# Kernel tuning notes

Measured on AMD Instinct MI355X. Metric: run time of the kernel, lower is better.

Reference implementation:

```python
import jax, jax.numpy as jnp
import numpy as np

B, L, LH, D, H = 32, 512, 2048, 1024, 4
DK = D // H  # dot-attn head dim
NEG = -1e9


def _ln(x, g, b, eps=1e-5):
    m = x.mean(-1, keepdims=True)
    v = ((x - m) ** 2).mean(-1, keepdims=True)
    return (x - m) / jnp.sqrt(v + eps) * g + b


def setup_inputs() -> dict:
    key = jax.random.key(0)
    ks = jax.random.split(key, 16)
    s = 0.05
    inp = {
        "seq_emb": jax.random.normal(ks[0], (B, L, D), jnp.float32),
        "seq_mask": jnp.ones((B, L), jnp.float32),
        "his_seq_emb": jax.random.normal(ks[1], (B, LH, D), jnp.float32),
        "his_seq_mask": jnp.ones((B, LH), jnp.float32),
        # dot-product MHA (bias=True)
        "sa_wq": jax.random.normal(ks[2], (D, D), jnp.float32) * s,
        "sa_bq": jnp.zeros((D,), jnp.float32),
        "sa_wk": jax.random.normal(ks[3], (D, D), jnp.float32) * s,
        "sa_bk": jnp.zeros((D,), jnp.float32),
        "sa_wv": jax.random.normal(ks[4], (D, D), jnp.float32) * s,
        "sa_bv": jnp.zeros((D,), jnp.float32),
        "sa_wo": jax.random.normal(ks[5], (D, D), jnp.float32) * s,
        "sa_bo": jnp.zeros((D,), jnp.float32),
        # short LayerNorm
        "sn_g": jnp.ones((D,), jnp.float32),
        "sn_b": jnp.zeros((D,), jnp.float32),
        # additive MHA (h=1, bias=False)
        "aa_wq": jax.random.normal(ks[6], (D, D), jnp.float32) * s,
        "aa_wk": jax.random.normal(ks[7], (D, D), jnp.float32) * s,
        "aa_wv": jax.random.normal(ks[8], (D, D), jnp.float32) * s,
        "aa_wo": jax.random.normal(ks[9], (D, D), jnp.float32) * s,
        "aa_wa": jax.random.normal(ks[10], (D,), jnp.float32) * s,
        # long LayerNorm
        "ln_g": jnp.ones((D,), jnp.float32),
        "ln_b": jnp.zeros((D,), jnp.float32),
    }
    return inp


def reference(seq_emb, seq_mask, his_seq_emb, his_seq_mask,
              sa_wq, sa_bq, sa_wk, sa_bk, sa_wv, sa_bv, sa_wo, sa_bo,
              sn_g, sn_b, aa_wq, aa_wk, aa_wv, aa_wo, aa_wa, ln_g, ln_b):
    # ---- dot-product self attention over seq_emb (dropout = eval/no-op) ----
    def split_heads(x):  # (B,L,D) -> (B,H,L,DK)
        return x.reshape(B, -1, H, DK).transpose(0, 2, 1, 3)

    q = split_heads(seq_emb @ sa_wq + sa_bq)
    k = split_heads(seq_emb @ sa_wk + sa_bk)
    v = split_heads(seq_emb @ sa_wv + sa_bv)
    scores = jnp.einsum('bhqd,bhkd->bhqk', q, k) / jnp.sqrt(jnp.float32(DK))
    scores = jnp.where(seq_mask[:, None, None, :] == 0, NEG, scores)
    p_attn = jax.nn.softmax(scores, axis=-1)  # (B,H,L,L)
    ctx = jnp.einsum('bhqk,bhkd->bhqd', p_attn, v)
    ctx = ctx.transpose(0, 2, 1, 3).reshape(B, L, D)
    sa_out = ctx @ sa_wo + sa_bo

    poi_attn = _ln(sa_out, sn_g, sn_b) * seq_mask[:, :, None]
    poi_hidden = poi_attn.mean(axis=1, keepdims=True)  # (B,1,D)

    # ---- additive (Bahdanau) attention, h=1, Lq=1 ----
    aq = poi_hidden @ aa_wq        # (B,1,D)
    ak = his_seq_emb @ aa_wk       # (B,LH,D)
    av = his_seq_emb @ aa_wv       # (B,LH,D)
    feats = jnp.tanh(aq[:, :, None, :] + ak[:, None, :, :])  # (B,1,LH,D)
    a_scores = jnp.einsum('bqkd,d->bqk', feats, aa_wa)        # (B,1,LH)
    a_scores = jnp.where(his_seq_mask[:, None, :] == 0, NEG, a_scores)
    a_w = jax.nn.softmax(a_scores, axis=-1)
    a_ctx = jnp.einsum('bqk,bkd->bqd', a_w, av)               # (B,1,D)
    aa_out = a_ctx @ aa_wo

    his_poi_hidden = poi_hidden + _ln(aa_out, ln_g, ln_b)     # (B,1,D)

    attn_weight = p_attn[:, 0, :, :]                          # (B,L,L)
    seq_hidden = jnp.concatenate([poi_hidden, his_poi_hidden], axis=-1)[:, 0, :]  # (B,2D)
    return seq_hidden, attn_weight
```

## Files before the change

### kernel.cpp

```cpp
#include <hip/hip_runtime.h>

#define NEGV (-1000000000.0f)

typedef __attribute__((ext_vector_type(8))) short sh8;
typedef __attribute__((ext_vector_type(4))) short sh4;
typedef __attribute__((ext_vector_type(8))) __bf16 bf16x8;
typedef __attribute__((ext_vector_type(4))) float f32x4;

__device__ __forceinline__ float b2f(unsigned short u) {
  unsigned v = ((unsigned)u) << 16;
  return __builtin_bit_cast(float, v);
}
__device__ __forceinline__ unsigned short f2b(float f) {
  unsigned x = __builtin_bit_cast(unsigned, f);
  unsigned r = (x + 0x7fffu + ((x >> 16) & 1u)) >> 16;
  return (unsigned short)r;
}
__device__ __forceinline__ void g2l16(const void* g, void* l) {
  __builtin_amdgcn_global_load_lds((const __attribute__((address_space(1))) unsigned int*)g,
                                   (__attribute__((address_space(3))) unsigned int*)l, 16, 0, 0);
}
__device__ __forceinline__ f32x4 mfma16(bf16x8 a, bf16x8 b, f32x4 c) {
  return __builtin_amdgcn_mfma_f32_16x16x32_bf16(a, b, c, 0, 0, 0);
}
__device__ __forceinline__ float fast_tanh(float x) {
  x = fminf(fmaxf(x, -15.f), 15.f);
  float e = __expf(2.f * x);
  return (e - 1.f) / (e + 1.f);
}

__global__ void cvt_bf16(const float* __restrict__ src, unsigned short* __restrict__ dst, int n4) {
  int i = blockIdx.x * blockDim.x + threadIdx.x;
  int stride = gridDim.x * blockDim.x;
  for (; i < n4; i += stride) {
    float4 v = ((const float4*)src)[i];
    sh4 o;
    o[0] = (short)f2b(v.x); o[1] = (short)f2b(v.y);
    o[2] = (short)f2b(v.z); o[3] = (short)f2b(v.w);
    ((sh4*)dst)[i] = o;
  }
}

__global__ void tcvt(const float* __restrict__ src, unsigned short* __restrict__ dst) {
  __shared__ float tile[64][65];
  int bx = blockIdx.x, by = blockIdx.y;
  int tx = threadIdx.x & 63, ty = threadIdx.x >> 6;
#pragma unroll
  for (int i = 0; i < 16; ++i) {
    int r = i * 4 + ty;
    tile[r][tx] = src[(size_t)(by * 64 + r) * 1024 + bx * 64 + tx];
  }
  __syncthreads();
#pragma unroll
  for (int i = 0; i < 16; ++i) {
    int r = i * 4 + ty;
    dst[(size_t)(bx * 64 + r) * 1024 + by * 64 + tx] = f2b(tile[tx][r]);
  }
}

template<int EPI>
__global__ __launch_bounds__(256, 2)
void gemm128(const unsigned short* __restrict__ A, const unsigned short* __restrict__ Bt,
             const float* __restrict__ bias, unsigned short* __restrict__ C,
             const float* __restrict__ aq, const float* __restrict__ wa,
             float* __restrict__ sc)
{
  __shared__ unsigned short ldsA[128 * 32];
  __shared__ unsigned short ldsB[128 * 32];
  const int tid = threadIdx.x;
  const int w = tid >> 6, l = tid & 63;
  const int wr = w >> 1, wc = w & 1;
  const int lr = l & 15, lk8 = (l >> 4) * 8;
  const int wg = blockIdx.x;
  const int cpx = gridDim.x >> 3;
  const int wgid = (wg & 7) * cpx + (wg >> 3);
  const int bx = wgid & 7, by = wgid >> 3;
  const int m0 = by * 128;
  const int n0 = bx * 128;

  f32x4 acc[4][4] = {};

  const int srow = tid >> 2;
  const int scol = (tid & 3) * 8;
  const unsigned short* gA0 = A + (size_t)(m0 + srow) * 1024 + scol;
  const unsigned short* gB0 = Bt + (size_t)(n0 + srow) * 1024 + scol;
  unsigned short* lA = &ldsA[w * 512];
  unsigned short* lB = &ldsB[w * 512];

  for (int kt = 0; kt < 32; ++kt) {
    const int k0 = kt * 32;
    g2l16(gA0 + k0, lA);
    g2l16(gA0 + 64 * 1024 + k0, lA + 2048);
    g2l16(gB0 + k0, lB);
    g2l16(gB0 + 64 * 1024 + k0, lB + 2048);
    __syncthreads();
    bf16x8 af[4], bf[4];
#pragma unroll
    for (int i = 0; i < 4; ++i)
      af[i] = *(const bf16x8*)&ldsA[(wr * 64 + i * 16 + lr) * 32 + lk8];
#pragma unroll
    for (int j = 0; j < 4; ++j)
      bf[j] = *(const bf16x8*)&ldsB[(wc * 64 + j * 16 + lr) * 32 + lk8];
#pragma unroll
    for (int i = 0; i < 4; ++i)
#pragma unroll
      for (int j = 0; j < 4; ++j)
        acc[i][j] = mfma16(af[i], bf[j], acc[i][j]);
    __syncthreads();
  }

  if (EPI == 0) {
#pragma unroll
    for (int j = 0; j < 4; ++j) {
      int col = n0 + wc * 64 + j * 16 + lr;
      float bv = bias[col];
#pragma unroll
      for (int i = 0; i < 4; ++i) {
        int rowb = m0 + wr * 64 + i * 16 + (l >> 4) * 4;
#pragma unroll
        for (int r = 0; r < 4; ++r)
          C[(size_t)(rowb + r) * 1024 + col] = f2b(acc[i][j][r] + bv);
      }
    }
  } else if (EPI == 1) {
#pragma unroll
    for (int j = 0; j < 4; ++j) {
      int col = n0 + wc * 64 + j * 16 + lr;
      float bv = bias[col];
      int h = col >> 8, d = col & 255;
#pragma unroll
      for (int i = 0; i < 4; ++i) {
        int rowb = m0 + wr * 64 + i * 16 + (l >> 4) * 4;
        int bb = rowb >> 9, ll = rowb & 511;
        size_t base = ((size_t)(bb * 4 + h) * 256 + d) * 512 + ll;
#pragma unroll
        for (int r = 0; r < 4; ++r)
          C[base + r] = f2b(acc[i][j][r] + bv);
      }
    }
  } else {
    const int bb = m0 >> 11;
#pragma unroll
    for (int i = 0; i < 4; ++i) {
      float rp[4] = {0.f, 0.f, 0.f, 0.f};
#pragma unroll
      for (int j = 0; j < 4; ++j) {
        int col = n0 + wc * 64 + j * 16 + lr;
        float wav = wa[col];
        float aqv = aq[bb * 1024 + col];
#pragma unroll
        for (int r = 0; r < 4; ++r)
          rp[r] += wav * fast_tanh(acc[i][j][r] + aqv);
      }
#pragma unroll
      for (int off = 1; off < 16; off <<= 1)
#pragma unroll
        for (int r = 0; r < 4; ++r)
          rp[r] += __shfl_xor(rp[r], off, 64);
      if (lr == 0) {
        int rowb = m0 + wr * 64 + i * 16 + (l >> 4) * 4;
#pragma unroll
        for (int r = 0; r < 4; ++r)
          atomicAdd(&sc[rowb + r], rp[r]);
      }
    }
  }
}

__global__ __launch_bounds__(256, 4)
void attn_kernel(const unsigned short* __restrict__ q, const unsigned short* __restrict__ k,
                 const unsigned short* __restrict__ vT, const float* __restrict__ seq_mask,
                 unsigned short* __restrict__ ctx, float* __restrict__ attn_out)
{
  __shared__ char smem[34304];
  unsigned short* Qs = (unsigned short*)smem;
  unsigned short* Ps = (unsigned short*)smem;
  float* redm = (float*)(smem + 33280);
  float* reds = (float*)(smem + 33792);
  const int t = threadIdx.x, w = t >> 6, l = t & 63;
  const int lr = l & 15, g = l >> 4, lk8 = g * 8;
  const int wg = blockIdx.x;
  const int wgid = (wg & 7) * 256 + (wg >> 3);
  const int qt = wgid & 15, bh = wgid >> 4;
  const int h = bh & 3, b = bh >> 2;
  const int l0 = qt * 32;

  for (int idx = t; idx < 32 * 32; idx += 256) {
    int r = idx >> 5, ch = (idx & 31) * 8;
    *(sh8*)&Qs[r * 264 + ch] =
        *(const sh8*)&q[((size_t)(b * 512 + l0 + r)) * 1024 + h * 256 + ch];
  }
  __syncthreads();

  f32x4 accs[2][8] = {};
  const unsigned short* kbase = k + ((size_t)b * 512) * 1024 + h * 256;
#pragma unroll
  for (int ds = 0; ds < 8; ++ds) {
    int d0 = ds * 32;
    bf16x8 a0 = *(const bf16x8*)&Qs[lr * 264 + d0 + lk8];
    bf16x8 a1 = *(const bf16x8*)&Qs[(16 + lr) * 264 + d0 + lk8];
#pragma unroll
    for (int j = 0; j < 8; ++j) {
      int kj = w * 128 + j * 16 + lr;
      bf16x8 bb = *(const bf16x8*)&kbase[(size_t)kj * 1024 + d0 + lk8];
      accs[0][j] = mfma16(a0, bb, accs[0][j]);
      accs[1][j] = mfma16(a1, bb, accs[1][j]);
    }
  }

#pragma unroll
  for (int j = 0; j < 8; ++j) {
    int col = w * 128 + j * 16 + lr;
    float mv = seq_mask[b * 512 + col];
    bool msk = (mv == 0.f);
#pragma unroll
    for (int i = 0; i < 2; ++i)
#pragma unroll
      for (int r = 0; r < 4; ++r)
        accs[i][j][r] = msk ? NEGV : accs[i][j][r] * 0.0625f;
  }

  float mx[2][4], sm[2][4];
#pragma unroll
  for (int i = 0; i < 2; ++i)
#pragma unroll
    for (int r = 0; r < 4; ++r) {
      float m = accs[i][0][r];
#pragma unroll
      for (int j = 1; j < 8; ++j) m = fmaxf(m, accs[i][j][r]);
      mx[i][r] = m;
    }
#pragma unroll
  for (int off = 1; off < 16; off <<= 1)
#pragma unroll
    for (int i = 0; i < 2; ++i)
#pragma unroll
      for (int r = 0; r < 4; ++r)
        mx[i][r] = fmaxf(mx[i][r], __shfl_xor(mx[i][r], off, 64));
  if (lr == 0) {
#pragma unroll
    for (int i = 0; i < 2; ++i)
#pragma unroll
      for (int r = 0; r < 4; ++r)
        redm[w * 32 + i * 16 + g * 4 + r] = mx[i][r];
  }
  __syncthreads();
#pragma unroll
  for (int i = 0; i < 2; ++i)
#pragma unroll
    for (int r = 0; r < 4; ++r) {
      int row = i * 16 + g * 4 + r;
      mx[i][r] = fmaxf(fmaxf(redm[row], redm[32 + row]),
                       fmaxf(redm[64 + row], redm[96 + row]));
      sm[i][r] = 0.f;
    }

#pragma unroll
  for (int i = 0; i < 2; ++i)
#pragma unroll
    for (int j = 0; j < 8; ++j)
#pragma unroll
      for (int r = 0; r < 4; ++r) {
        float p = __expf(accs[i][j][r] - mx[i][r]);
        accs[i][j][r] = p;
        sm[i][r] += p;
      }
#pragma unroll
  for (int off = 1; off < 16; off <<= 1)
#pragma unroll
    for (int i = 0; i < 2; ++i)
#pragma unroll
      for (int r = 0; r < 4; ++r)
        sm[i][r] += __shfl_xor(sm[i][r], off, 64);
  if (lr == 0) {
#pragma unroll
    for (int i = 0; i < 2; ++i)
#pragma unroll
      for (int r = 0; r < 4; ++r)
        reds[w * 32 + i * 16 + g * 4 + r] = sm[i][r];
  }
  __syncthreads();
#pragma unroll
  for (int i = 0; i < 2; ++i)
#pragma unroll
    for (int r = 0; r < 4; ++r) {
      int row = i * 16 + g * 4 + r;
      float s = reds[row] + reds[32 + row] + reds[64 + row] + reds[96 + row];
      sm[i][r] = 1.f / s;
    }

#pragma unroll
  for (int i = 0; i < 2; ++i)
#pragma unroll
    for (int j = 0; j < 8; ++j) {
      int col = w * 128 + j * 16 + lr;
#pragma unroll
      for (int r = 0; r < 4; ++r) {
        int row = i * 16 + g * 4 + r;
        float pn = accs[i][j][r] * sm[i][r];
        Ps[row * 520 + col] = f2b(pn);
        if (h == 0)
          attn_out[((size_t)(b * 512 + l0 + row)) * 512 + col] = pn;
      }
    }
  __syncthreads();

  f32x4 acco[2][4] = {};
  const unsigned short* vbase = vT + ((size_t)(b * 4 + h)) * 256 * 512;
#pragma unroll
  for (int ks = 0; ks < 16; ++ks) {
    int kj0 = ks * 32;
    bf16x8 a0 = *(const bf16x8*)&Ps[lr * 520 + kj0 + lk8];
    bf16x8 a1 = *(const bf16x8*)&Ps[(16 + lr) * 520 + kj0 + lk8];
#pragma unroll
    for (int j = 0; j < 4; ++j) {
      int d = w * 64 + j * 16 + lr;
      bf16x8 bb = *(const bf16x8*)&vbase[(size_t)d * 512 + kj0 + lk8];
      acco[0][j] = mfma16(a0, bb, acco[0][j]);
      acco[1][j] = mfma16(a1, bb, acco[1][j]);
    }
  }
#pragma unroll
  for (int i = 0; i < 2; ++i)
#pragma unroll
    for (int j = 0; j < 4; ++j) {
      int col = w * 64 + j * 16 + lr;
#pragma unroll
      for (int r = 0; r < 4; ++r) {
        int row = i * 16 + g * 4 + r;
        ctx[((size_t)(b * 512 + l0 + row)) * 1024 + h * 256 + col] = f2b(acco[i][j][r]);
      }
    }
}

__global__ __launch_bounds__(256)
void ln_mean(const unsigned short* __restrict__ sa, const float* __restrict__ g,
             const float* __restrict__ bt, const float* __restrict__ mask,
             float* __restrict__ poi_sum)
{
  const int b = blockIdx.y, ch = blockIdx.x;
  const int t = threadIdx.x, w = t >> 6, l = t & 63;
  float gg[16], bb[16];
#pragma unroll
  for (int j = 0; j < 16; ++j) { gg[j] = g[l * 16 + j]; bb[j] = bt[l * 16 + j]; }
  float accv[16];
#pragma unroll
  for (int j = 0; j < 16; ++j) accv[j] = 0.f;
  for (int rr = 0; rr < 16; ++rr) {
    int row = ch * 64 + w * 16 + rr;
    const unsigned short* rp = sa + ((size_t)(b * 512 + row)) * 1024 + l * 16;
    float x[16];
    sh8 v0 = *(const sh8*)rp;
    sh8 v1 = *(const sh8*)(rp + 8);
#pragma unroll
    for (int j = 0; j < 8; ++j) {
      x[j] = b2f((unsigned short)v0[j]);
      x[8 + j] = b2f((unsigned short)v1[j]);
    }
    float s = 0.f, s2 = 0.f;
#pragma unroll
    for (int j = 0; j < 16; ++j) { s += x[j]; s2 += x[j] * x[j]; }
#pragma unroll
    for (int off = 1; off < 64; off <<= 1) {
      s += __shfl_xor(s, off, 64);
      s2 += __shfl_xor(s2, off, 64);
    }
    float mean = s * (1.f / 1024.f);
    float var = s2 * (1.f / 1024.f) - mean * mean;
    float rinv = rsqrtf(var + 1e-5f);
    float mk = mask[b * 512 + row];
#pragma unroll
    for (int j = 0; j < 16; ++j) accv[j] += ((x[j] - mean) * rinv * gg[j] + bb[j]) * mk;
  }
#pragma unroll
  for (int j = 0; j < 16; ++j) atomicAdd(&poi_sum[b * 1024 + l * 16 + j], accv[j]);
}

__global__ void finalize_poi(const float* __restrict__ ps, float* __restrict__ poi) {
  int i = blockIdx.x * 256 + threadIdx.x;
  if (i < 32 * 1024) poi[i] = ps[i] * (1.f / 512.f);
}

__global__ __launch_bounds__(256)
void gemv32(const float* __restrict__ in, const float* __restrict__ W, float* __restrict__ out)
{
  const int b = blockIdx.y;
  const int n = blockIdx.x * 256 + threadIdx.x;
  const float* ib = in + b * 1024;
  float acc = 0.f;
  for (int d = 0; d < 1024; d += 4) {
    acc += ib[d]     * W[(size_t)d * 1024 + n]
         + ib[d + 1] * W[(size_t)(d + 1) * 1024 + n]
         + ib[d + 2] * W[(size_t)(d + 2) * 1024 + n]
         + ib[d + 3] * W[(size_t)(d + 3) * 1024 + n];
  }
  out[b * 1024 + n] = acc;
}

__global__ __launch_bounds__(256)
void softmax_his(float* __restrict__ sc, const float* __restrict__ mask)
{
  __shared__ float red[4];
  const int b = blockIdx.x, t = threadIdx.x, w = t >> 6, l = t & 63;
  float v[8];
  float mx = -3.0e38f;
#pragma unroll
  for (int i = 0; i < 8; ++i) {
    int kk = t + i * 256;
    float s = (mask[b * 2048 + kk] == 0.f) ? NEGV : sc[b * 2048 + kk];
    v[i] = s;
    mx = fmaxf(mx, s);
  }
#pragma unroll
  for (int off = 1; off < 64; off <<= 1) mx = fmaxf(mx, __shfl_xor(mx, off, 64));
  if (l == 0) red[w] = mx;
  __syncthreads();
  mx = fmaxf(fmaxf(red[0], red[1]), fmaxf(red[2], red[3]));
  float sum = 0.f;
#pragma unroll
  for (int i = 0; i < 8; ++i) { v[i] = __expf(v[i] - mx); sum += v[i]; }
#pragma unroll
  for (int off = 1; off < 64; off <<= 1) sum += __shfl_xor(sum, off, 64);
  __syncthreads();
  if (l == 0) red[w] = sum;
  __syncthreads();
  sum = red[0] + red[1] + red[2] + red[3];
  float inv = 1.f / sum;
#pragma unroll
  for (int i = 0; i < 8; ++i) sc[b * 2048 + t + i * 256] = v[i] * inv;
}

__global__ __launch_bounds__(256)
void hw_kernel(const float* __restrict__ aw, const unsigned short* __restrict__ his,
               float* __restrict__ hw)
{
  const int b = blockIdx.y, kc = blockIdx.x, t = threadIdx.x;
  const int cb = t * 4;
  float a0 = 0.f, a1 = 0.f, a2 = 0.f, a3 = 0.f;
  for (int kk = 0; kk < 256; ++kk) {
    int k = kc * 256 + kk;
    float wg = aw[b * 2048 + k];
    sh4 vv = *(const sh4*)&his[((size_t)(b * 2048 + k)) * 1024 + cb];
    a0 += wg * b2f((unsigned short)vv[0]);
    a1 += wg * b2f((unsigned short)vv[1]);
    a2 += wg * b2f((unsigned short)vv[2]);
    a3 += wg * b2f((unsigned short)vv[3]);
  }
  atomicAdd(&hw[b * 1024 + cb + 0], a0);
  atomicAdd(&hw[b * 1024 + cb + 1], a1);
  atomicAdd(&hw[b * 1024 + cb + 2], a2);
  atomicAdd(&hw[b * 1024 + cb + 3], a3);
}

__global__ __launch_bounds__(256)
void final_kernel(const float* __restrict__ aa_out, const float* __restrict__ g,
                  const float* __restrict__ bt, const float* __restrict__ poi,
                  float* __restrict__ out)
{
  __shared__ float r1[4], r2[4];
  const int b = blockIdx.x, t = threadIdx.x, w = t >> 6, l = t & 63;
  float x[4];
#pragma unroll
  for (int j = 0; j < 4; ++j) x[j] = aa_out[b * 1024 + t * 4 + j];
  float s = 0.f, s2 = 0.f;
#pragma unroll
  for (int j = 0; j < 4; ++j) { s += x[j]; s2 += x[j] * x[j]; }
#pragma unroll
  for (int off = 1; off < 64; off <<= 1) {
    s += __shfl_xor(s, off, 64);
    s2 += __shfl_xor(s2, off, 64);
  }
  if (l == 0) { r1[w] = s; r2[w] = s2; }
  __syncthreads();
  s = r1[0] + r1[1] + r1[2] + r1[3];
  s2 = r2[0] + r2[1] + r2[2] + r2[3];
  float mean = s * (1.f / 1024.f);
  float var = s2 * (1.f / 1024.f) - mean * mean;
  float rinv = rsqrtf(var + 1e-5f);
#pragma unroll
  for (int j = 0; j < 4; ++j) {
    int c = t * 4 + j;
    float lnv = (x[j] - mean) * rinv * g[c] + bt[c];
    float pv = poi[b * 1024 + c];
    out[b * 2048 + c] = pv;
    out[b * 2048 + 1024 + c] = pv + lnv;
  }
}

extern "C" void kernel_launch(void* const* d_in, const int* in_sizes, int n_in,
                              void* d_out, int out_size, void* d_ws, size_t ws_size,
                              hipStream_t stream)
{
  const float* seq_emb  = (const float*)d_in[0];
  const float* seq_mask = (const float*)d_in[1];
  const float* his_emb  = (const float*)d_in[2];
  const float* his_mask = (const float*)d_in[3];
  const float* sa_wq = (const float*)d_in[4];
  const float* sa_bq = (const float*)d_in[5];
  const float* sa_wk = (const float*)d_in[6];
  const float* sa_bk = (const float*)d_in[7];
  const float* sa_wv = (const float*)d_in[8];
  const float* sa_bv = (const float*)d_in[9];
  const float* sa_wo = (const float*)d_in[10];
  const float* sa_bo = (const float*)d_in[11];
  const float* sn_g  = (const float*)d_in[12];
  const float* sn_b  = (const float*)d_in[13];
  const float* aa_wq = (const float*)d_in[14];
  const float* aa_wk = (const float*)d_in[15];
  const float* aa_wv = (const float*)d_in[16];
  const float* aa_wo = (const float*)d_in[17];
  const float* aa_wa = (const float*)d_in[18];
  const float* ln_g  = (const float*)d_in[19];
  const float* ln_b  = (const float*)d_in[20];
  float* out = (float*)d_out;

  char* p = (char*)d_ws;
  size_t off = 0;
  auto alloc = [&](size_t bytes) -> void* {
    void* r = p + off;
    off += (bytes + 255) & ~(size_t)255;
    return r;
  };
  unsigned short* seqb = (unsigned short*)alloc((size_t)16384 * 1024 * 2);
  unsigned short* hisb = (unsigned short*)alloc((size_t)65536 * 1024 * 2);
  unsigned short* wqT  = (unsigned short*)alloc((size_t)1024 * 1024 * 2);
  unsigned short* wkT  = (unsigned short*)alloc((size_t)1024 * 1024 * 2);
  unsigned short* wvT  = (unsigned short*)alloc((size_t)1024 * 1024 * 2);
  unsigned short* woT  = (unsigned short*)alloc((size_t)1024 * 1024 * 2);
  unsigned short* awkT = (unsigned short*)alloc((size_t)1024 * 1024 * 2);
  unsigned short* qb   = (unsigned short*)alloc((size_t)16384 * 1024 * 2);
  unsigned short* kb   = (unsigned short*)alloc((size_t)16384 * 1024 * 2);
  unsigned short* vTb  = (unsigned short*)alloc((size_t)16384 * 1024 * 2);
  unsigned short* ctxb = (unsigned short*)alloc((size_t)16384 * 1024 * 2);
  unsigned short* saob = (unsigned short*)alloc((size_t)16384 * 1024 * 2);
  float* poi_sum = (float*)alloc((size_t)32 * 1024 * 4);
  float* poi     = (float*)alloc((size_t)32 * 1024 * 4);
  float* aqb     = (float*)alloc((size_t)32 * 1024 * 4);
  float* ascore  = (float*)alloc((size_t)32 * 2048 * 4);
  float* hwb     = (float*)alloc((size_t)32 * 1024 * 4);
  float* actx    = (float*)alloc((size_t)32 * 1024 * 4);
  float* aaout   = (float*)alloc((size_t)32 * 1024 * 4);
  if (off > ws_size) return;

  hipMemsetAsync(poi_sum, 0, (size_t)32 * 1024 * 4, stream);
  hipMemsetAsync(ascore, 0, (size_t)32 * 2048 * 4, stream);
  hipMemsetAsync(hwb, 0, (size_t)32 * 1024 * 4, stream);

  cvt_bf16<<<2048, 256, 0, stream>>>(seq_emb, seqb, 16384 * 1024 / 4);
  cvt_bf16<<<2048, 256, 0, stream>>>(his_emb, hisb, 65536 * 1024 / 4);
  dim3 tg(16, 16);
  tcvt<<<tg, 256, 0, stream>>>(sa_wq, wqT);
  tcvt<<<tg, 256, 0, stream>>>(sa_wk, wkT);
  tcvt<<<tg, 256, 0, stream>>>(sa_wv, wvT);
  tcvt<<<tg, 256, 0, stream>>>(sa_wo, woT);
  tcvt<<<tg, 256, 0, stream>>>(aa_wk, awkT);

  gemm128<0><<<1024, 256, 0, stream>>>(seqb, wqT, sa_bq, qb, nullptr, nullptr, nullptr);
  gemm128<0><<<1024, 256, 0, stream>>>(seqb, wkT, sa_bk, kb, nullptr, nullptr, nullptr);
  gemm128<1><<<1024, 256, 0, stream>>>(seqb, wvT, sa_bv, vTb, nullptr, nullptr, nullptr);

  attn_kernel<<<2048, 256, 0, stream>>>(qb, kb, vTb, seq_mask, ctxb, out + 65536);

  gemm128<0><<<1024, 256, 0, stream>>>(ctxb, woT, sa_bo, saob, nullptr, nullptr, nullptr);
  ln_mean<<<dim3(8, 32), 256, 0, stream>>>(saob, sn_g, sn_b, seq_mask, poi_sum);
  finalize_poi<<<128, 256, 0, stream>>>(poi_sum, poi);
  gemv32<<<dim3(4, 32), 256, 0, stream>>>(poi, aa_wq, aqb);

  gemm128<2><<<4096, 256, 0, stream>>>(hisb, awkT, nullptr, nullptr, aqb, aa_wa, ascore);
  softmax_his<<<32, 256, 0, stream>>>(ascore, his_mask);
  hw_kernel<<<dim3(8, 32), 256, 0, stream>>>(ascore, hisb, hwb);
  gemv32<<<dim3(4, 32), 256, 0, stream>>>(hwb, aa_wv, actx);
  gemv32<<<dim3(4, 32), 256, 0, stream>>>(actx, aa_wo, aaout);
  final_kernel<<<32, 256, 0, stream>>>(aaout, ln_g, ln_b, poi, out);
}
```

Baseline: 823.2 us.

## Replace 128x128 GEMM with pipelined 256x256 tile kernel and fuse QKV projections

Replaces the 128x128-tile, 256-thread GEMM with a 256x256-tile, 512-thread kernel that keeps a 4-stage LDS ring, loading two k-steps ahead. Loads are interleaved with MFMA phases using split barriers, explicit waitcnt and setprio. The Q/K/V weights are concatenated so one launch computes all three projections. The goal is more data reuse per tile, hiding global-load latency, and fewer launches. In exchange it uses 128KB of LDS at one block per CU, and the hand-managed vmcnt and barrier logic is fragile.

```diff
diff --git a/kernel.cpp b/kernel.cpp
--- a/kernel.cpp
+++ b/kernel.cpp
@@ -59,93 +59,154 @@
 }
 
 template<int EPI>
-__global__ __launch_bounds__(256, 2)
-void gemm128(const unsigned short* __restrict__ A, const unsigned short* __restrict__ Bt,
-             const float* __restrict__ bias, unsigned short* __restrict__ C,
+__global__ __launch_bounds__(512, 1)
+void gemm256(const unsigned short* __restrict__ A, const unsigned short* __restrict__ Bt,
+             int nbx,
+             const float* __restrict__ b0, const float* __restrict__ b1,
+             const float* __restrict__ b2,
+             unsigned short* __restrict__ O0, unsigned short* __restrict__ O1,
+             unsigned short* __restrict__ O2,
              const float* __restrict__ aq, const float* __restrict__ wa,
              float* __restrict__ sc)
 {
-  __shared__ unsigned short ldsA[128 * 32];
-  __shared__ unsigned short ldsB[128 * 32];
+  __shared__ char lds[131072];
   const int tid = threadIdx.x;
   const int w = tid >> 6, l = tid & 63;
-  const int wr = w >> 1, wc = w & 1;
-  const int lr = l & 15, lk8 = (l >> 4) * 8;
+  const int wm = w >> 2, wn = w & 3;
+  const int lr = l & 15, g = l >> 4;
+  const int kg16 = g * 16;
+
   const int wg = blockIdx.x;
   const int cpx = gridDim.x >> 3;
   const int wgid = (wg & 7) * cpx + (wg >> 3);
-  const int bx = wgid & 7, by = wgid >> 3;
-  const int m0 = by * 128;
-  const int n0 = bx * 128;
-
-  f32x4 acc[4][4] = {};
-
-  const int srow = tid >> 2;
-  const int scol = (tid & 3) * 8;
-  const unsigned short* gA0 = A + (size_t)(m0 + srow) * 1024 + scol;
-  const unsigned short* gB0 = Bt + (size_t)(n0 + srow) * 1024 + scol;
-  unsigned short* lA = &ldsA[w * 512];
-  unsigned short* lB = &ldsB[w * 512];
-
+  const int bx = wgid % nbx, by = wgid / nbx;
+  const size_t m0 = (size_t)by * 256;
+  const int n0 = bx * 256;
+
+  f32x4 acc[8][4] = {};
+
+  const int srow = tid >> 2, sk = (tid & 3) * 8;
+  const unsigned short* gA = A + (m0 + srow) * 1024 + sk;
+  const unsigned short* gB = Bt + ((size_t)n0 + srow) * 1024 + sk;
+  char* const sbase = lds + w * 1024;
+
+  const int aoff = (wm * 128 + lr) * 64 + kg16;
+  const int boff = 16384 + (wn * 64 + lr) * 64 + kg16;
+
+#pragma unroll
+  for (int p = 0; p < 2; ++p) {
+    const unsigned short* a = gA + p * 32;
+    const unsigned short* b = gB + p * 32;
+    char* base = sbase + (p << 15);
+    g2l16(a, base);
+    g2l16(a + 128 * 1024, base + 8192);
+    g2l16(b, base + 16384);
+    g2l16(b + 128 * 1024, base + 24576);
+  }
+  asm volatile("s_waitcnt vmcnt(4)" ::: "memory");
+  __builtin_amdgcn_s_barrier();
+
+#pragma unroll 1
   for (int kt = 0; kt < 32; ++kt) {
-    const int k0 = kt * 32;
-    g2l16(gA0 + k0, lA);
-    g2l16(gA0 + 64 * 1024 + k0, lA + 2048);
-    g2l16(gB0 + k0, lB);
-    g2l16(gB0 + 64 * 1024 + k0, lB + 2048);
-    __syncthreads();
+    const char* pb = lds + ((kt & 3) << 15);
+    char* nb = sbase + (((kt + 2) & 3) << 15);
     bf16x8 af[4], bf[4];
-#pragma unroll
-    for (int i = 0; i < 4; ++i)
-      af[i] = *(const bf16x8*)&ldsA[(wr * 64 + i * 16 + lr) * 32 + lk8];
-#pragma unroll
-    for (int j = 0; j < 4; ++j)
-      bf[j] = *(const bf16x8*)&ldsB[(wc * 64 + j * 16 + lr) * 32 + lk8];
+
+    if (kt < 30) {
+      const unsigned short* a = gA + (kt + 2) * 32;
+      g2l16(a, nb);
+      g2l16(a + 128 * 1024, nb + 8192);
+    }
+#pragma unroll
+    for (int j = 0; j < 4; ++j) bf[j] = *(const bf16x8*)(pb + boff + j * 1024);
+#pragma unroll
+    for (int i = 0; i < 4; ++i) af[i] = *(const bf16x8*)(pb + aoff + i * 1024);
+    __builtin_amdgcn_s_barrier();
+    asm volatile("s_waitcnt lgkmcnt(0)" ::: "memory");
+    __builtin_amdgcn_sched_barrier(0);
+    __builtin_amdgcn_s_setprio(1);
 #pragma unroll
     for (int i = 0; i < 4; ++i)
 #pragma unroll
       for (int j = 0; j < 4; ++j)
         acc[i][j] = mfma16(af[i], bf[j], acc[i][j]);
-    __syncthreads();
+    __builtin_amdgcn_s_setprio(0);
+    __builtin_amdgcn_s_barrier();
+
+    if (kt < 30) {
+      const unsigned short* b = gB + (kt + 2) * 32;
+      g2l16(b, nb + 16384);
+      g2l16(b + 128 * 1024, nb + 24576);
+    }
+#pragma unroll
+    for (int i = 0; i < 4; ++i) af[i] = *(const bf16x8*)(pb + aoff + (4 + i) * 1024);
+    __builtin_amdgcn_s_barrier();
+    asm volatile("s_waitcnt lgkmcnt(0)" ::: "memory");
+    __builtin_amdgcn_sched_barrier(0);
+    __builtin_amdgcn_s_setprio(1);
+#pragma unroll
+    for (int i = 0; i < 4; ++i)
+#pragma unroll
+      for (int j = 0; j < 4; ++j)
+        acc[4 + i][j] = mfma16(af[i], bf[j], acc[4 + i][j]);
+    __builtin_amdgcn_s_setprio(0);
+    if (kt < 30) {
+      asm volatile("s_waitcnt vmcnt(4)" ::: "memory");
+    } else if (kt == 30) {
+      asm volatile("s_waitcnt vmcnt(0)" ::: "memory");
+    }
+    __builtin_amdgcn_s_barrier();
   }
 
   if (EPI == 0) {
 #pragma unroll
     for (int j = 0; j < 4; ++j) {
-      int col = n0 + wc * 64 + j * 16 + lr;
-      float bv = bias[col];
-#pragma unroll
-      for (int i = 0; i < 4; ++i) {
-        int rowb = m0 + wr * 64 + i * 16 + (l >> 4) * 4;
+      int col = n0 + wn * 64 + j * 16 + lr;
+      float bv = b0[col];
+#pragma unroll
+      for (int i = 0; i < 8; ++i) {
+        size_t rowb = m0 + wm * 128 + i * 16 + g * 4;
 #pragma unroll
         for (int r = 0; r < 4; ++r)
-          C[(size_t)(rowb + r) * 1024 + col] = f2b(acc[i][j][r] + bv);
+          O0[(rowb + r) * 1024 + col] = f2b(acc[i][j][r] + bv);
       }
     }
   } else if (EPI == 1) {
 #pragma unroll
     for (int j = 0; j < 4; ++j) {
-      int col = n0 + wc * 64 + j * 16 + lr;
-      float bv = bias[col];
-      int h = col >> 8, d = col & 255;
-#pragma unroll
-      for (int i = 0; i < 4; ++i) {
-        int rowb = m0 + wr * 64 + i * 16 + (l >> 4) * 4;
-        int bb = rowb >> 9, ll = rowb & 511;
-        size_t base = ((size_t)(bb * 4 + h) * 256 + d) * 512 + ll;
-#pragma unroll
-        for (int r = 0; r < 4; ++r)
-          C[base + r] = f2b(acc[i][j][r] + bv);
+      int col3 = n0 + wn * 64 + j * 16 + lr;
+      int part = col3 >> 10, c = col3 & 1023;
+      float bv = (part == 0) ? b0[c] : (part == 1) ? b1[c] : b2[c];
+      if (part < 2) {
+        unsigned short* O = part == 0 ? O0 : O1;
+#pragma unroll
+        for (int i = 0; i < 8; ++i) {
+          size_t rowb = m0 + wm * 128 + i * 16 + g * 4;
+#pragma unroll
+          for (int r = 0; r < 4; ++r)
+            O[(rowb + r) * 1024 + c] = f2b(acc[i][j][r] + bv);
+        }
+      } else {
+        int h = c >> 8, d = c & 255;
+#pragma unroll
+        for (int i = 0; i < 8; ++i) {
+          size_t row = m0 + wm * 128 + i * 16 + g * 4;
+          int bb = (int)(row >> 9), ll = (int)(row & 511);
+          size_t base = ((size_t)(bb * 4 + h) * 256 + d) * 512 + ll;
+#pragma unroll
+          for (int r = 0; r < 4; ++r)
+            O2[base + r] = f2b(acc[i][j][r] + bv);
+        }
       }
     }
   } else {
-    const int bb = m0 >> 11;
-#pragma unroll
-    for (int i = 0; i < 4; ++i) {
+    const int bb = (int)(m0 >> 11);
+#pragma unroll
+    for (int i = 0; i < 8; ++i) {
       float rp[4] = {0.f, 0.f, 0.f, 0.f};
 #pragma unroll
       for (int j = 0; j < 4; ++j) {
-        int col = n0 + wc * 64 + j * 16 + lr;
+        int col = n0 + wn * 64 + j * 16 + lr;
         float wav = wa[col];
         float aqv = aq[bb * 1024 + col];
 #pragma unroll
@@ -158,7 +219,7 @@
         for (int r = 0; r < 4; ++r)
           rp[r] += __shfl_xor(rp[r], off, 64);
       if (lr == 0) {
-        int rowb = m0 + wr * 64 + i * 16 + (l >> 4) * 4;
+        size_t rowb = m0 + wm * 128 + i * 16 + g * 4;
 #pragma unroll
         for (int r = 0; r < 4; ++r)
           atomicAdd(&sc[rowb + r], rp[r]);
@@ -523,9 +584,7 @@
   };
   unsigned short* seqb = (unsigned short*)alloc((size_t)16384 * 1024 * 2);
   unsigned short* hisb = (unsigned short*)alloc((size_t)65536 * 1024 * 2);
-  unsigned short* wqT  = (unsigned short*)alloc((size_t)1024 * 1024 * 2);
-  unsigned short* wkT  = (unsigned short*)alloc((size_t)1024 * 1024 * 2);
-  unsigned short* wvT  = (unsigned short*)alloc((size_t)1024 * 1024 * 2);
+  unsigned short* wcat = (unsigned short*)alloc((size_t)3072 * 1024 * 2);
   unsigned short* woT  = (unsigned short*)alloc((size_t)1024 * 1024 * 2);
   unsigned short* awkT = (unsigned short*)alloc((size_t)1024 * 1024 * 2);
   unsigned short* qb   = (unsigned short*)alloc((size_t)16384 * 1024 * 2);
@@ -549,24 +608,25 @@
   cvt_bf16<<<2048, 256, 0, stream>>>(seq_emb, seqb, 16384 * 1024 / 4);
   cvt_bf16<<<2048, 256, 0, stream>>>(his_emb, hisb, 65536 * 1024 / 4);
   dim3 tg(16, 16);
-  tcvt<<<tg, 256, 0, stream>>>(sa_wq, wqT);
-  tcvt<<<tg, 256, 0, stream>>>(sa_wk, wkT);
-  tcvt<<<tg, 256, 0, stream>>>(sa_wv, wvT);
+  tcvt<<<tg, 256, 0, stream>>>(sa_wq, wcat);
+  tcvt<<<tg, 256, 0, stream>>>(sa_wk, wcat + (size_t)1024 * 1024);
+  tcvt<<<tg, 256, 0, stream>>>(sa_wv, wcat + (size_t)2048 * 1024);
   tcvt<<<tg, 256, 0, stream>>>(sa_wo, woT);
   tcvt<<<tg, 256, 0, stream>>>(aa_wk, awkT);
 
-  gemm128<0><<<1024, 256, 0, stream>>>(seqb, wqT, sa_bq, qb, nullptr, nullptr, nullptr);
-  gemm128<0><<<1024, 256, 0, stream>>>(seqb, wkT, sa_bk, kb, nullptr, nullptr, nullptr);
-  gemm128<1><<<1024, 256, 0, stream>>>(seqb, wvT, sa_bv, vTb, nullptr, nullptr, nullptr);
+  gemm256<1><<<768, 512, 0, stream>>>(seqb, wcat, 12, sa_bq, sa_bk, sa_bv,
+                                      qb, kb, vTb, nullptr, nullptr, nullptr);
 
   attn_kernel<<<2048, 256, 0, stream>>>(qb, kb, vTb, seq_mask, ctxb, out + 65536);
 
-  gemm128<0><<<1024, 256, 0, stream>>>(ctxb, woT, sa_bo, saob, nullptr, nullptr, nullptr);
+  gemm256<0><<<256, 512, 0, stream>>>(ctxb, woT, 4, sa_bo, nullptr, nullptr,
+                                      saob, nullptr, nullptr, nullptr, nullptr, nullptr);
   ln_mean<<<dim3(8, 32), 256, 0, stream>>>(saob, sn_g, sn_b, seq_mask, poi_sum);
   finalize_poi<<<128, 256, 0, stream>>>(poi_sum, poi);
   gemv32<<<dim3(4, 32), 256, 0, stream>>>(poi, aa_wq, aqb);
 
-  gemm128<2><<<4096, 256, 0, stream>>>(hisb, awkT, nullptr, nullptr, aqb, aa_wa, ascore);
+  gemm256<2><<<1024, 512, 0, stream>>>(hisb, awkT, 4, nullptr, nullptr, nullptr,
+                                       nullptr, nullptr, nullptr, aqb, aa_wa, ascore);
   softmax_his<<<32, 256, 0, stream>>>(ascore, his_mask);
   hw_kernel<<<dim3(8, 32), 256, 0, stream>>>(ascore, hisb, hwb);
   gemv32<<<dim3(4, 32), 256, 0, stream>>>(hwb, aa_wv, actx);
```

Result: no change. 822.5 us (-0.1%).
